# Kernel optimization log

Measured on AMD Instinct MI355X. Metric: run time of the kernel, lower is better.

## Reference

```python
import jax, jax.numpy as jnp
import numpy as np

B, S, IN, OUT, L, R = 2, 8192, 2048, 2048, 4, 32


def setup_inputs() -> dict:
    key = jax.random.key(0)
    ks = jax.random.split(key, 6)
    return {
        "x": jax.random.normal(ks[0], (B, S, IN), dtype=jnp.float32),
        "weight": jax.random.normal(ks[1], (OUT, IN), dtype=jnp.float32) * 0.02,
        "bias": jax.random.normal(ks[2], (OUT,), dtype=jnp.float32) * 0.02,
        "downs": jax.random.normal(ks[3], (L, R, IN), dtype=jnp.float32) * 0.02,
        "ups": jax.random.normal(ks[4], (L, OUT, R), dtype=jnp.float32) * 0.02,
        "scales": jax.random.uniform(ks[5], (L,), dtype=jnp.float32),
    }


def reference(x, weight, bias, downs, ups, scales):
    # Base linear: y = x @ W.T + b
    y = jnp.einsum("bsi,oi->bso", x, weight) + bias
    # Low-rank LoRA deltas, grouped across adapters:
    # tmp[b,s,l,r] = x @ down_l.T ; delta = sum_l scale_l * tmp_l @ up_l.T
    tmp = jnp.einsum("bsi,lri->bslr", x, downs)  # [B,S,L,R]
    tmp = tmp * scales[None, None, :, None]       # fold per-adapter scale
    delta = jnp.einsum("bslr,lor->bso", tmp, ups)  # [B,S,OUT]
    return y + delta
```

## Files before the change

kernel.cpp:

```cpp
#include <hip/hip_runtime.h>

#define M_DIM 16384
#define N_DIM 2048
#define K_DIM 2048
#define L_AD 4
#define R_AD 32

typedef __bf16 bf16_t;
typedef bf16_t bf16x8 __attribute__((ext_vector_type(8)));
typedef bf16_t bf16x4 __attribute__((ext_vector_type(4)));
typedef float f32x4 __attribute__((ext_vector_type(4)));

#define BM 128
#define BN 128
#define BK 64
#define SA 72

__device__ __forceinline__ void async_load16(const void* g, void* l) {
  __builtin_amdgcn_global_load_lds(
      (const __attribute__((address_space(1))) unsigned int*)g,
      (__attribute__((address_space(3))) unsigned int*)l, 16, 0, 0);
}

__global__ __launch_bounds__(256) void build_weff_kernel(
    const float* __restrict__ W, const float* __restrict__ downs,
    const float* __restrict__ ups, const float* __restrict__ scales,
    bf16_t* __restrict__ weff) {
  __shared__ float up_s[64 * 129];
  __shared__ float down_s[128 * 64];
  const int t = threadIdx.x;
  const int n0 = blockIdx.y * 64;
  const int k0 = blockIdx.x * 64;

  for (int l = 0; l < L_AD; ++l) {
    const float sc = scales[l];
    const float* up_l = ups + (size_t)l * N_DIM * R_AD;
    #pragma unroll
    for (int j = 0; j < 8; ++j) {
      int flat = j * 256 + t;
      int nl = flat >> 5, r = flat & 31;
      up_s[nl * 129 + l * 32 + r] = sc * up_l[(size_t)(n0 + nl) * R_AD + r];
    }
  }
  #pragma unroll
  for (int j = 0; j < 32; ++j) {
    int flat = j * 256 + t;
    int lr = flat >> 6, kk = flat & 63;
    down_s[lr * 64 + kk] = downs[(size_t)lr * K_DIM + k0 + kk];
  }
  __syncthreads();

  const int tn = t >> 4, tk = t & 15;
  float acc[4][4] = {};
  for (int lr = 0; lr < L_AD * R_AD; ++lr) {
    f32x4 b = *(const f32x4*)&down_s[lr * 64 + tk * 4];
    #pragma unroll
    for (int u = 0; u < 4; ++u) {
      float a = up_s[(tn * 4 + u) * 129 + lr];
      #pragma unroll
      for (int v = 0; v < 4; ++v) acc[u][v] += a * b[v];
    }
  }
  #pragma unroll
  for (int u = 0; u < 4; ++u) {
    int n = n0 + tn * 4 + u;
    f32x4 wv = *(const f32x4*)&W[(size_t)n * K_DIM + k0 + tk * 4];
    bf16x4 o;
    #pragma unroll
    for (int v = 0; v < 4; ++v) o[v] = (bf16_t)(acc[u][v] + wv[v]);
    *(bf16x4*)&weff[(size_t)n * K_DIM + k0 + tk * 4] = o;
  }
}

__global__ __launch_bounds__(256) void lora_gemm_kernel(
    const float* __restrict__ X, const bf16_t* __restrict__ Wb,
    const float* __restrict__ bias, float* __restrict__ out) {
  __shared__ __align__(16) bf16_t As[BM * SA];
  __shared__ __align__(16) bf16_t Bs[BN * BK];

  const int t = threadIdx.x;
  const int lane = t & 63;
  const int wv = t >> 6;
  const int wm = wv >> 1, wn = wv & 1;
  const int col = lane & 15, quad = lane >> 4;
  const int m0 = blockIdx.y * BM;
  const int n0 = blockIdx.x * BN;

  const int srow = t >> 3;
  const int soct = t & 7;

  f32x4 acc[4][4] = {};

  float bn[4];
  #pragma unroll
  for (int j = 0; j < 4; ++j) bn[j] = bias[n0 + wn * 64 + j * 16 + col];

  for (int kt = 0; kt < K_DIM / BK; ++kt) {
    const int kg = kt * BK;
    #pragma unroll
    for (int j = 0; j < 4; ++j) {
      int n = j * 32 + srow;
      int c = soct ^ (n & 7);
      const bf16_t* src = Wb + (size_t)(n0 + n) * K_DIM + kg + c * 8;
      async_load16(src, &Bs[(size_t)(j * 256 + t) * 8]);
    }
    #pragma unroll
    for (int j = 0; j < 4; ++j) {
      int m = j * 32 + srow;
      const f32x4* src = (const f32x4*)(X + (size_t)(m0 + m) * K_DIM + kg + soct * 8);
      f32x4 lo = src[0], hi = src[1];
      bf16x8 v;
      v[0] = (bf16_t)lo[0]; v[1] = (bf16_t)lo[1];
      v[2] = (bf16_t)lo[2]; v[3] = (bf16_t)lo[3];
      v[4] = (bf16_t)hi[0]; v[5] = (bf16_t)hi[1];
      v[6] = (bf16_t)hi[2]; v[7] = (bf16_t)hi[3];
      *(bf16x8*)&As[m * SA + soct * 8] = v;
    }
    __syncthreads();

    #pragma unroll
    for (int ks = 0; ks < 2; ++ks) {
      bf16x8 af[4], bfr[4];
      #pragma unroll
      for (int i = 0; i < 4; ++i)
        af[i] = *(const bf16x8*)&As[(wm * 64 + i * 16 + col) * SA + ks * 32 + quad * 8];
      #pragma unroll
      for (int j = 0; j < 4; ++j) {
        int n = wn * 64 + j * 16 + col;
        int p = (ks * 4 + quad) ^ (n & 7);
        bfr[j] = *(const bf16x8*)&Bs[n * BK + p * 8];
      }
      #pragma unroll
      for (int i = 0; i < 4; ++i) {
        #pragma unroll
        for (int j = 0; j < 4; ++j)
          acc[i][j] = __builtin_amdgcn_mfma_f32_16x16x32_bf16(af[i], bfr[j], acc[i][j], 0, 0, 0);
      }
    }
    __syncthreads();
  }

  #pragma unroll
  for (int i = 0; i < 4; ++i) {
    #pragma unroll
    for (int r = 0; r < 4; ++r) {
      int m = m0 + wm * 64 + i * 16 + quad * 4 + r;
      float* orow = out + (size_t)m * N_DIM + n0 + wn * 64 + col;
      #pragma unroll
      for (int j = 0; j < 4; ++j)
        orow[j * 16] = acc[i][j][r] + bn[j];
    }
  }
}

extern "C" void kernel_launch(void* const* d_in, const int* in_sizes, int n_in,
                              void* d_out, int out_size, void* d_ws, size_t ws_size,
                              hipStream_t stream) {
  const float* x      = (const float*)d_in[0];
  const float* weight = (const float*)d_in[1];
  const float* bias   = (const float*)d_in[2];
  const float* downs  = (const float*)d_in[3];
  const float* ups    = (const float*)d_in[4];
  const float* scales = (const float*)d_in[5];
  float* out = (float*)d_out;
  bf16_t* weff = (bf16_t*)d_ws;

  dim3 g1(K_DIM / 64, N_DIM / 64);
  build_weff_kernel<<<g1, 256, 0, stream>>>(weight, downs, ups, scales, weff);

  dim3 g2(N_DIM / BN, M_DIM / BM);
  lora_gemm_kernel<<<g2, 256, 0, stream>>>(x, weff, bias, out);
}
```

Before: 458.0 us.

## Pre-convert X to bf16 and async-load both GEMM operands into LDS

Adds a separate pass that converts the fp32 activations to bf16 in the workspace. The main GEMM can then stage both A and B tiles with direct global-to-LDS async loads and an XOR-swizzled layout, instead of loading fp32 X through registers and converting it inside the K loop. This removes the repeated fp32 reads and conversion work that every N-tile did before, and halves the bytes fetched for A. In exchange it adds a full extra read/write pass over X and needs extra workspace, with the old path kept as a fallback when the workspace is too small.

```diff
diff --git a/kernel.cpp b/kernel.cpp
--- a/kernel.cpp
+++ b/kernel.cpp
@@ -14,12 +14,24 @@
 #define BM 128
 #define BN 128
 #define BK 64
-#define SA 72
 
 __device__ __forceinline__ void async_load16(const void* g, void* l) {
   __builtin_amdgcn_global_load_lds(
       (const __attribute__((address_space(1))) unsigned int*)g,
       (__attribute__((address_space(3))) unsigned int*)l, 16, 0, 0);
+}
+
+__global__ __launch_bounds__(256) void convert_x_kernel(
+    const float* __restrict__ X, bf16_t* __restrict__ Xb) {
+  const size_t base = ((size_t)blockIdx.x * 256 + threadIdx.x) * 8;
+  f32x4 lo = *(const f32x4*)(X + base);
+  f32x4 hi = *(const f32x4*)(X + base + 4);
+  bf16x8 v;
+  v[0] = (bf16_t)lo[0]; v[1] = (bf16_t)lo[1];
+  v[2] = (bf16_t)lo[2]; v[3] = (bf16_t)lo[3];
+  v[4] = (bf16_t)hi[0]; v[5] = (bf16_t)hi[1];
+  v[6] = (bf16_t)hi[2]; v[7] = (bf16_t)hi[3];
+  *(bf16x8*)(Xb + base) = v;
 }
 
 __global__ __launch_bounds__(256) void build_weff_kernel(
@@ -72,10 +84,10 @@
   }
 }
 
-__global__ __launch_bounds__(256) void lora_gemm_kernel(
-    const float* __restrict__ X, const bf16_t* __restrict__ Wb,
+__global__ __launch_bounds__(256) void gemm_bf16_kernel(
+    const bf16_t* __restrict__ Xb, const bf16_t* __restrict__ Wb,
     const float* __restrict__ bias, float* __restrict__ out) {
-  __shared__ __align__(16) bf16_t As[BM * SA];
+  __shared__ __align__(16) bf16_t As[BM * BK];
   __shared__ __align__(16) bf16_t Bs[BN * BK];
 
   const int t = threadIdx.x;
@@ -99,10 +111,83 @@
     const int kg = kt * BK;
     #pragma unroll
     for (int j = 0; j < 4; ++j) {
+      int row = j * 32 + srow;
+      int c = soct ^ (row & 7);
+      async_load16(Wb + (size_t)(n0 + row) * K_DIM + kg + c * 8,
+                   &Bs[(size_t)(row * 8 + soct) * 8]);
+      async_load16(Xb + (size_t)(m0 + row) * K_DIM + kg + c * 8,
+                   &As[(size_t)(row * 8 + soct) * 8]);
+    }
+    __syncthreads();
+
+    #pragma unroll
+    for (int ks = 0; ks < 2; ++ks) {
+      bf16x8 af[4], bfr[4];
+      #pragma unroll
+      for (int i = 0; i < 4; ++i) {
+        int row = wm * 64 + i * 16 + col;
+        int p = (ks * 4 + quad) ^ (row & 7);
+        af[i] = *(const bf16x8*)&As[row * BK + p * 8];
+      }
+      #pragma unroll
+      for (int j = 0; j < 4; ++j) {
+        int row = wn * 64 + j * 16 + col;
+        int p = (ks * 4 + quad) ^ (row & 7);
+        bfr[j] = *(const bf16x8*)&Bs[row * BK + p * 8];
+      }
+      #pragma unroll
+      for (int i = 0; i < 4; ++i) {
+        #pragma unroll
+        for (int j = 0; j < 4; ++j)
+          acc[i][j] = __builtin_amdgcn_mfma_f32_16x16x32_bf16(af[i], bfr[j], acc[i][j], 0, 0, 0);
+      }
+    }
+    __syncthreads();
+  }
+
+  #pragma unroll
+  for (int i = 0; i < 4; ++i) {
+    #pragma unroll
+    for (int r = 0; r < 4; ++r) {
+      int m = m0 + wm * 64 + i * 16 + quad * 4 + r;
+      float* orow = out + (size_t)m * N_DIM + n0 + wn * 64 + col;
+      #pragma unroll
+      for (int j = 0; j < 4; ++j)
+        orow[j * 16] = acc[i][j][r] + bn[j];
+    }
+  }
+}
+
+#define SA 72
+__global__ __launch_bounds__(256) void lora_gemm_fallback(
+    const float* __restrict__ X, const bf16_t* __restrict__ Wb,
+    const float* __restrict__ bias, float* __restrict__ out) {
+  __shared__ __align__(16) bf16_t As[BM * SA];
+  __shared__ __align__(16) bf16_t Bs[BN * BK];
+
+  const int t = threadIdx.x;
+  const int lane = t & 63;
+  const int wv = t >> 6;
+  const int wm = wv >> 1, wn = wv & 1;
+  const int col = lane & 15, quad = lane >> 4;
+  const int m0 = blockIdx.y * BM;
+  const int n0 = blockIdx.x * BN;
+  const int srow = t >> 3;
+  const int soct = t & 7;
+
+  f32x4 acc[4][4] = {};
+  float bn[4];
+  #pragma unroll
+  for (int j = 0; j < 4; ++j) bn[j] = bias[n0 + wn * 64 + j * 16 + col];
+
+  for (int kt = 0; kt < K_DIM / BK; ++kt) {
+    const int kg = kt * BK;
+    #pragma unroll
+    for (int j = 0; j < 4; ++j) {
       int n = j * 32 + srow;
       int c = soct ^ (n & 7);
-      const bf16_t* src = Wb + (size_t)(n0 + n) * K_DIM + kg + c * 8;
-      async_load16(src, &Bs[(size_t)(j * 256 + t) * 8]);
+      async_load16(Wb + (size_t)(n0 + n) * K_DIM + kg + c * 8,
+                   &Bs[(size_t)(j * 256 + t) * 8]);
     }
     #pragma unroll
     for (int j = 0; j < 4; ++j) {
@@ -163,11 +248,21 @@
   const float* ups    = (const float*)d_in[4];
   const float* scales = (const float*)d_in[5];
   float* out = (float*)d_out;
+
+  const size_t weff_bytes = (size_t)N_DIM * K_DIM * 2;
+  const size_t xb_bytes   = (size_t)M_DIM * K_DIM * 2;
   bf16_t* weff = (bf16_t*)d_ws;
 
   dim3 g1(K_DIM / 64, N_DIM / 64);
   build_weff_kernel<<<g1, 256, 0, stream>>>(weight, downs, ups, scales, weff);
 
   dim3 g2(N_DIM / BN, M_DIM / BM);
-  lora_gemm_kernel<<<g2, 256, 0, stream>>>(x, weff, bias, out);
-}
+  if (ws_size >= weff_bytes + xb_bytes) {
+    bf16_t* xb = (bf16_t*)((char*)d_ws + weff_bytes);
+    const size_t n_elem = (size_t)M_DIM * K_DIM;
+    convert_x_kernel<<<(unsigned)(n_elem / (256 * 8)), 256, 0, stream>>>(x, xb);
+    gemm_bf16_kernel<<<g2, 256, 0, stream>>>(xb, weff, bias, out);
+  } else {
+    lora_gemm_fallback<<<g2, 256, 0, stream>>>(x, weff, bias, out);
+  }
+}
```

Result: faster. 405.8 us (-11.4%).
